# Kernel tuning notes

Hardware: AMD Instinct MI355X
Metric: run time of the kernel (lower is better)

The kernel has to match this reference:

```python
import jax, jax.numpy as jnp
import numpy as np

HOP = 160
FFT = 1024
NUM_LABELS = 72
B, T = 4, 240000


def setup_inputs() -> dict:
    key = jax.random.key(0)
    k1, _ = jax.random.split(key)
    lbl = jax.random.randint(k1, (B, T), 0, NUM_LABELS, dtype=jnp.int64 if jax.config.jax_enable_x64 else jnp.int32)
    weight = jnp.ones((FFT,), dtype=jnp.float32)  # frozen all-ones conv kernel
    return {"lbl": lbl, "weight": weight}


def reference(lbl, weight):
    pad = FFT // 2
    # ReflectionPad1d on the label stream: [B, T] -> [B, L], L = T + 2*pad
    x = jnp.pad(lbl, ((0, 0), (pad, pad)), mode="reflect")
    L = x.shape[-1]
    # one-hot scatter: [B, NUM_LABELS, L] fp32 (dominant memory traffic)
    onehot = jax.nn.one_hot(x, NUM_LABELS, axis=1, dtype=jnp.float32)
    # sliding-window sum of size FFT, stride HOP, per label channel.
    # Conv2d(1,1,(1,FFT),stride=(1,HOP)) over [B,1,C,L] == 1D conv applied to each
    # (batch, label) row independently: fold C into the batch dim.
    y = jax.lax.conv_general_dilated(
        onehot.reshape(B * NUM_LABELS, 1, L),
        weight.reshape(1, 1, FFT),
        window_strides=(HOP,),
        padding="VALID",
        dimension_numbers=("NCH", "OIH", "NCH"),
    )  # [B*C, 1, n_out]
    n_out = y.shape[-1]
    counts = y.reshape(B, NUM_LABELS, n_out)
    # majority label per window
    return jnp.argmax(counts, axis=1)
```

## Files before the change

kernel.cpp:

```cpp
#include <hip/hip_runtime.h>

#define HOP 160
#define FFT 1024
#define PAD (FFT / 2)
#define NUM_LABELS 72
#define BATCH 4
#define T 240000
#define NOUT 1501
#define R 8
#define NBLK ((NOUT + R - 1) / R)

__global__ __launch_bounds__(256) void label_window_argmax(
    const int* __restrict__ lbl, int* __restrict__ out)
{
    __shared__ int hist[4][NUM_LABELS];
    __shared__ int keys[NUM_LABELS];

    const int tid  = threadIdx.x;
    const int wave = tid >> 6;
    const int lane = tid & 63;

    for (int i = tid; i < 4 * NUM_LABELS; i += 256)
        ((int*)hist)[i] = 0;

    const int b  = blockIdx.y;
    const int w0 = blockIdx.x * R;
    const int* __restrict__ row = lbl + b * T;

    auto refl = [&](int j) {
        j = (j < 0) ? -j : j;
        j = (j >= T) ? (2 * (T - 1) - j) : j;
        return j;
    };

    __syncthreads();

    {
        const int s = w0 * HOP - PAD;
#pragma unroll
        for (int k = 0; k < 4; ++k) {
            const int lab = row[refl(s + tid + k * 256)];
            atomicAdd(&hist[wave][lab], 1);
        }
    }

    for (int step = 0; step < R; ++step) {
        const int w = w0 + step;
        if (w >= NOUT) break;
        __syncthreads();

        if (tid < NUM_LABELS) {
            const int tot = hist[0][tid] + hist[1][tid] + hist[2][tid] + hist[3][tid];
            keys[tid] = (tot << 7) | (NUM_LABELS - 1 - tid);
        }
        __syncthreads();

        if (wave == 0) {
            int k = keys[lane];
            if (lane < NUM_LABELS - 64)
                k = max(k, keys[64 + lane]);
#pragma unroll
            for (int off = 32; off; off >>= 1)
                k = max(k, __shfl_xor(k, off, 64));
            if (lane == 0)
                out[b * NOUT + w] = NUM_LABELS - 1 - (k & 127);
        }

        if (step + 1 < R && w + 1 < NOUT) {
            const int s = w * HOP - PAD;
            if (tid < HOP) {
                const int lab = row[refl(s + tid)];
                atomicAdd(&hist[wave][lab], -1);
            }
            const int t2 = tid - (256 - HOP);
            if (t2 >= 0) {
                const int lab = row[refl(s + FFT + t2)];
                atomicAdd(&hist[wave][lab], 1);
            }
        }
    }
}

extern "C" void kernel_launch(void* const* d_in, const int* in_sizes, int n_in,
                              void* d_out, int out_size, void* d_ws, size_t ws_size,
                              hipStream_t stream) {
    const int* lbl = (const int*)d_in[0];
    int* out = (int*)d_out;

    dim3 grid(NBLK, BATCH);
    label_window_argmax<<<grid, 256, 0, stream>>>(lbl, out);
}
```

Measured before the change: 61.64 us.

## Assign one window per wave with int4 loads and sub-histograms

```diff
diff --git a/kernel.cpp b/kernel.cpp
--- a/kernel.cpp
+++ b/kernel.cpp
@@ -7,78 +7,77 @@
 #define BATCH 4
 #define T 240000
 #define NOUT 1501
-#define R 8
-#define NBLK ((NOUT + R - 1) / R)
+#define WPB 4
+#define NSUB 4
+#define HSTRIDE 72
 
 __global__ __launch_bounds__(256) void label_window_argmax(
     const int* __restrict__ lbl, int* __restrict__ out)
 {
-    __shared__ int hist[4][NUM_LABELS];
-    __shared__ int keys[NUM_LABELS];
+    __shared__ int hist[WPB][NSUB][HSTRIDE];
 
     const int tid  = threadIdx.x;
     const int wave = tid >> 6;
     const int lane = tid & 63;
+    const int sub  = lane >> 4;
 
-    for (int i = tid; i < 4 * NUM_LABELS; i += 256)
-        ((int*)hist)[i] = 0;
+    int* hbase = &hist[wave][0][0];
+    for (int i = lane; i < NSUB * HSTRIDE; i += 64)
+        hbase[i] = 0;
 
-    const int b  = blockIdx.y;
-    const int w0 = blockIdx.x * R;
+    const int gid = blockIdx.x * WPB + wave;
+    const int b   = gid / NOUT;
+    const int w   = gid - b * NOUT;
     const int* __restrict__ row = lbl + b * T;
-
-    auto refl = [&](int j) {
-        j = (j < 0) ? -j : j;
-        j = (j >= T) ? (2 * (T - 1) - j) : j;
-        return j;
-    };
+    const int s = w * HOP - PAD;
 
     __syncthreads();
 
-    {
-        const int s = w0 * HOP - PAD;
+    int* hsub = &hist[wave][sub][0];
+    if (s >= 0 && s + FFT <= T) {
+        const int4* p = reinterpret_cast<const int4*>(row + s);
 #pragma unroll
         for (int k = 0; k < 4; ++k) {
-            const int lab = row[refl(s + tid + k * 256)];
-            atomicAdd(&hist[wave][lab], 1);
+            const int4 v = p[k * 64 + lane];
+            atomicAdd(&hsub[v.x], 1);
+            atomicAdd(&hsub[v.y], 1);
+            atomicAdd(&hsub[v.z], 1);
+            atomicAdd(&hsub[v.w], 1);
+        }
+    } else {
+        auto refl = [&](int j) {
+            j = (j < 0) ? -j : j;
+            j = (j >= T) ? (2 * (T - 1) - j) : j;
+            return j;
+        };
+#pragma unroll
+        for (int k = 0; k < 16; ++k) {
+            const int lab = row[refl(s + k * 64 + lane)];
+            atomicAdd(&hsub[lab], 1);
         }
     }
 
-    for (int step = 0; step < R; ++step) {
-        const int w = w0 + step;
-        if (w >= NOUT) break;
-        __syncthreads();
+    __syncthreads();
 
-        if (tid < NUM_LABELS) {
-            const int tot = hist[0][tid] + hist[1][tid] + hist[2][tid] + hist[3][tid];
-            keys[tid] = (tot << 7) | (NUM_LABELS - 1 - tid);
-        }
-        __syncthreads();
-
-        if (wave == 0) {
-            int k = keys[lane];
-            if (lane < NUM_LABELS - 64)
-                k = max(k, keys[64 + lane]);
+    int k0;
+    {
+        const int c0 = hist[wave][0][lane] + hist[wave][1][lane]
+                     + hist[wave][2][lane] + hist[wave][3][lane];
+        k0 = (c0 << 7) | (NUM_LABELS - 1 - lane);
+    }
+    int k1 = 0;
+    if (lane < NUM_LABELS - 64) {
+        const int l2 = 64 + lane;
+        const int c1 = hist[wave][0][l2] + hist[wave][1][l2]
+                     + hist[wave][2][l2] + hist[wave][3][l2];
+        k1 = (c1 << 7) | (NUM_LABELS - 1 - l2);
+    }
+    int k = max(k0, k1);
 #pragma unroll
-            for (int off = 32; off; off >>= 1)
-                k = max(k, __shfl_xor(k, off, 64));
-            if (lane == 0)
-                out[b * NOUT + w] = NUM_LABELS - 1 - (k & 127);
-        }
-
-        if (step + 1 < R && w + 1 < NOUT) {
-            const int s = w * HOP - PAD;
-            if (tid < HOP) {
-                const int lab = row[refl(s + tid)];
-                atomicAdd(&hist[wave][lab], -1);
-            }
-            const int t2 = tid - (256 - HOP);
-            if (t2 >= 0) {
-                const int lab = row[refl(s + FFT + t2)];
-                atomicAdd(&hist[wave][lab], 1);
-            }
-        }
-    }
+    for (int off = 32; off; off >>= 1)
+        k = max(k, __shfl_xor(k, off, 64));
+    if (lane == 0)
+        out[b * NOUT + w] = NUM_LABELS - 1 - (k & 127);
 }
 
 extern "C" void kernel_launch(void* const* d_in, const int* in_sizes, int n_in,
@@ -87,6 +86,7 @@
     const int* lbl = (const int*)d_in[0];
     int* out = (int*)d_out;
 
-    dim3 grid(NBLK, BATCH);
+    static_assert(WPB * ((BATCH * NOUT) / WPB) == BATCH * NOUT, "exact wave tiling");
+    dim3 grid((BATCH * NOUT) / WPB);
     label_window_argmax<<<grid, 256, 0, stream>>>(lbl, out);
 }
```

New measurement: 59.24 us. 3.9% less time.
